# Optimization experiments

Hardware: AMD Instinct MI355X
Metric: run time of the kernel (lower is better)

Reference implementation:

```python
import jax, jax.numpy as jnp
import numpy as np

B, N, IN_DIM, ATT_DIM = 2, 8192, 512, 512


def setup_inputs() -> dict:
    key = jax.random.key(0)
    k1, k2, k3, k4 = jax.random.split(key, 4)
    X = jax.random.normal(k1, (B, N, IN_DIM), dtype=jnp.float32)
    adj = jax.random.uniform(k2, (B, N, N), dtype=jnp.float32)
    mask = jnp.ones((B, N), dtype=jnp.float32)
    # Learned params (torch Linear stores W as (out,in); we store (in,out) for x @ W)
    Wqk = jax.random.normal(k3, (IN_DIM, 2 * ATT_DIM), dtype=jnp.float32) / np.sqrt(IN_DIM)
    Wv = jax.random.normal(k4, (IN_DIM, IN_DIM), dtype=jnp.float32) / np.sqrt(IN_DIM)
    return {"X": X, "adj": adj, "mask": mask, "Wqk": Wqk, "Wv": Wv}


def reference(X, adj, mask, Wqk, Wv):
    # q, k: (B, N, att_dim); v: (B, N, in_dim)
    qk = X @ Wqk
    q, k = jnp.split(qk, 2, axis=-1)
    v = X @ Wv
    att_dim = q.shape[-1]
    inv_scale = 1.0 / jnp.sqrt(jnp.float32(att_dim))
    # Original math: w_i = inv_scale * sum_j adj_ij * m_i * m_j * (q_i . k_j).
    # Since the rank-1 mask factors (m_i m_j), fold m_j into k and m_i into the row
    # score, avoiding a second materialized NxN tensor:
    k_m = k * mask[:, :, None]                       # (B, N, att_dim)
    agg = jnp.einsum("bij,bjd->bid", adj, k_m)       # (B, N, att_dim)
    w = inv_scale * mask * jnp.einsum("bid,bid->bi", q, agg)  # (B, N)
    # softmax over the bag dimension (dim=1), then scale v rows
    L = jax.nn.softmax(w, axis=1)[:, :, None] * v    # (B, N, in_dim)
    return L
```

## Files before the change

### kernel.cpp

```cpp
#include <hip/hip_runtime.h>
#include <math.h>

#define BB 2
#define NN 8192
#define DD 512

static const float INV_SCALE = 0.04419417382415922f;

typedef short s16x8 __attribute__((ext_vector_type(8)));
typedef unsigned short u16x8 __attribute__((ext_vector_type(8)));
typedef float f32x4 __attribute__((ext_vector_type(4)));

#define AS1 __attribute__((address_space(1)))
#define AS3 __attribute__((address_space(3)))

__device__ __forceinline__ unsigned short bfbits(__bf16 h) {
    return __builtin_bit_cast(unsigned short, h);
}

__device__ __forceinline__ float b2f(unsigned short u) {
    unsigned int x = (unsigned int)u << 16;
    return __builtin_bit_cast(float, x);
}

__device__ __forceinline__ void gll16(const void* g, void* l) {
    __builtin_amdgcn_global_load_lds((const AS1 unsigned int*)g, (AS3 unsigned int*)l, 16, 0, 0);
}

__device__ __forceinline__ f32x4 ntload4(const float* p) {
    return __builtin_nontemporal_load((const f32x4*)p);
}

__global__ __launch_bounds__(256) void convx_k(
    const float* __restrict__ X, unsigned short* __restrict__ Xhi,
    unsigned short* __restrict__ Xlo)
{
    long i = (long)blockIdx.x * 256 + threadIdx.x;
    float4 x = ((const float4*)X)[i];
    __bf16 h0 = (__bf16)x.x, h1 = (__bf16)x.y, h2 = (__bf16)x.z, h3 = (__bf16)x.w;
    ushort4 hi4 = make_ushort4(bfbits(h0), bfbits(h1), bfbits(h2), bfbits(h3));
    __bf16 l0 = (__bf16)(x.x - (float)h0), l1 = (__bf16)(x.y - (float)h1);
    __bf16 l2 = (__bf16)(x.z - (float)h2), l3 = (__bf16)(x.w - (float)h3);
    ushort4 lo4 = make_ushort4(bfbits(l0), bfbits(l1), bfbits(l2), bfbits(l3));
    ((ushort4*)Xhi)[i] = hi4;
    ((ushort4*)Xlo)[i] = lo4;
}

__global__ __launch_bounds__(256) void convw_k(
    const float* __restrict__ Wqk, const float* __restrict__ Wv,
    unsigned short* __restrict__ QTh, unsigned short* __restrict__ KTh,
    unsigned short* __restrict__ KTl, unsigned short* __restrict__ VTh)
{
    int i = blockIdx.x * 256 + threadIdx.x;
    if (i < 262144) {
        int n = i >> 9, k = i & 511;
        QTh[i] = bfbits((__bf16)Wqk[k * 1024 + n]);
    } else if (i < 524288) {
        int o = i - 262144; int n = o >> 9, k = o & 511;
        float val = Wqk[k * 1024 + 512 + n];
        __bf16 h = (__bf16)val;
        KTh[o] = bfbits(h);
        KTl[o] = bfbits((__bf16)(val - (float)h));
    } else {
        int o = i - 524288; int n = o >> 9, k = o & 511;
        VTh[o] = bfbits((__bf16)Wv[k * 512 + n]);
    }
}


template <int EPI, int NT>
__global__ __launch_bounds__(256, 4) void mfma_gemm(
    const unsigned short* __restrict__ A0, const unsigned short* __restrict__ A1,
    const unsigned short* __restrict__ B0, const unsigned short* __restrict__ B1,
    float* __restrict__ C, float* __restrict__ kmf,
    unsigned short* __restrict__ ubuf, const float* __restrict__ mask,
    int N, int K)
{
    constexpr int BK = 32;
    constexpr int TILE_SH = 128 * BK;

    __shared__ unsigned short Asm[2 * TILE_SH];
    __shared__ unsigned short Bsm[2 * TILE_SH];

    const int t = threadIdx.x;
    const int wv = t >> 6, lane = t & 63;
    const int wm = wv >> 1, wn = wv & 1;
    const long m0 = blockIdx.x * 128;
    const int n0 = blockIdx.y * 128;

    f32x4 acc[4][4];
#pragma unroll
    for (int i = 0; i < 4; ++i)
#pragma unroll
        for (int j = 0; j < 4; ++j) acc[i][j] = {0.f, 0.f, 0.f, 0.f};

    const int swz = ((lane & 3) ^ ((lane >> 3) & 3)) << 4;
    auto stageA = [&](int term, int k0, int buf) {
        const unsigned short* Ab = (term < 2) ? A0 : A1;
#pragma unroll
        for (int u = 0; u < 2; ++u) {
            int c = wv * 2 + u;
            int row = c * 16 + (lane >> 2);
            gll16((const char*)Ab + ((m0 + row) * (long)K + k0) * 2 + swz,
                  (char*)Asm + buf * (TILE_SH * 2) + c * 1024);
        }
    };
    auto stageB = [&](int term, int k0, int buf) {
        const unsigned short* Bb = (NT == 3 && term == 1) ? B1 : B0;
#pragma unroll
        for (int u = 0; u < 2; ++u) {
            int c = wv * 2 + u;
            int row = c * 16 + (lane >> 2);
            gll16((const char*)Bb + ((long)(n0 + row) * K + k0) * 2 + swz,
                  (char*)Bsm + buf * (TILE_SH * 2) + c * 1024);
        }
    };

    stageA(0, 0, 0);
    stageB(0, 0, 0);
    __syncthreads();

    const int NTILES = NT * (K / BK);
    int cur = 0, term = 0, k0 = 0;
    const int g = lane >> 4;

#pragma unroll 2
    for (int tt = 0; tt < NTILES; ++tt) {
        int k0n = k0 + BK, termn = term;
        if (k0n == K) { k0n = 0; ++termn; }
        const bool hasNext = (tt + 1 < NTILES);

        if (hasNext) {
            stageA(termn, k0n, cur ^ 1);
            stageB(termn, k0n, cur ^ 1);
        }

        s16x8 av[4], bv[4];
#pragma unroll
        for (int f = 0; f < 4; ++f) {
            int ra = wm * 64 + f * 16 + (lane & 15);
            int rb = wn * 64 + f * 16 + (lane & 15);
            av[f] = *(const s16x8*)(Asm + cur * TILE_SH + ra * BK
                     + ((g ^ ((ra >> 1) & 3)) << 3));
            bv[f] = *(const s16x8*)(Bsm + cur * TILE_SH + rb * BK
                     + ((g ^ ((rb >> 1) & 3)) << 3));
        }
#pragma unroll
        for (int fm = 0; fm < 4; ++fm)
#pragma unroll
            for (int fn = 0; fn < 4; ++fn)
                acc[fm][fn] = __builtin_amdgcn_mfma_f32_16x16x32_bf16(
                    av[fm], bv[fn], acc[fm][fn], 0, 0, 0);

        __syncthreads();
        cur ^= 1; term = termn; k0 = k0n;
    }

    const long rbase = m0 + wm * 64;
    const int cbase = n0 + wn * 64;

#pragma unroll
    for (int fm = 0; fm < 4; ++fm) {
        long rb = rbase + fm * 16 + ((lane >> 4) << 2);
#pragma unroll
        for (int fn = 0; fn < 4; ++fn) {
            int c = cbase + fn * 16 + (lane & 15);
            if constexpr (EPI == 0) {
#pragma unroll
                for (int j = 0; j < 4; ++j)
                    C[(rb + j) * (long)N + c] = acc[fm][fn][j];
            } else if constexpr (EPI == 1) {
#pragma unroll
                for (int j = 0; j < 4; ++j) {
                    float kv = acc[fm][fn][j] * mask[rb + j];
                    kmf [(rb + j) * 512L + c] = kv;
                    ubuf[(rb + j) * 512L + c] = bfbits((__bf16)kv);
                }
            } else {
#pragma unroll
                for (int j = 0; j < 4; ++j)
                    ubuf[(rb + j) * 512L + c] = bfbits((__bf16)acc[fm][fn][j]);
            }
        }
    }
}

__global__ __launch_bounds__(256, 5) void sq_gemm(
    const unsigned short* __restrict__ qh,
    const unsigned short* __restrict__ kmh,
    const float* __restrict__ adj,
    float* __restrict__ w)
{
    constexpr int BK = 32;
    constexpr int TILE_SH = 128 * BK;

    __shared__ __align__(16) char smem[32768];
    unsigned short* Asm = (unsigned short*)smem;
    unsigned short* Bsm = (unsigned short*)(smem + 16384);
    unsigned short* Sh = (unsigned short*)smem;

    const int t = threadIdx.x;
    const int wv = t >> 6, lane = t & 63;
    const int wm = wv >> 1, wn = wv & 1;

    const int bid = (int)blockIdx.x;
    const int xcd = bid & 7, s = bid >> 3;
    const int z = s >> 9, r = s & 511;
    const int jj = r & 7, ii = (r >> 3) & 7, jhi = r >> 6;
    const int i_tile = xcd * 8 + ii;
    const int j_tile = jhi * 8 + jj;

    const long m0 = (long)z * NN + (long)i_tile * 128;
    const int n0 = j_tile * 128;
    const unsigned short* Bz = kmh + (long)z * NN * 512;

    f32x4 acc[4][4];
#pragma unroll
    for (int i = 0; i < 4; ++i)
#pragma unroll
        for (int j = 0; j < 4; ++j) acc[i][j] = {0.f, 0.f, 0.f, 0.f};

    const int swz = ((lane & 3) ^ ((lane >> 3) & 3)) << 4;
    auto stageA = [&](int k0, int buf) {
#pragma unroll
        for (int u = 0; u < 2; ++u) {
            int c = wv * 2 + u;
            int row = c * 16 + (lane >> 2);
            gll16((const char*)qh + ((m0 + row) * 512L + k0) * 2 + swz,
                  (char*)Asm + buf * (TILE_SH * 2) + c * 1024);
        }
    };
    auto stageB = [&](int k0, int buf) {
#pragma unroll
        for (int u = 0; u < 2; ++u) {
            int c = wv * 2 + u;
            int row = c * 16 + (lane >> 2);
            gll16((const char*)Bz + ((long)(n0 + row) * 512 + k0) * 2 + swz,
                  (char*)Bsm + buf * (TILE_SH * 2) + c * 1024);
        }
    };

    stageA(0, 0);
    stageB(0, 0);
    __syncthreads();

    const int g = lane >> 4;
#pragma unroll 2
    for (int tt = 0; tt < 16; ++tt) {
        const int cur = tt & 1;
        const bool hasNext = (tt + 1 < 16);
        if (hasNext) {
            stageA((tt + 1) * BK, cur ^ 1);
            stageB((tt + 1) * BK, cur ^ 1);
        }

        s16x8 av[4], bv[4];
#pragma unroll
        for (int f = 0; f < 4; ++f) {
            int ra = wm * 64 + f * 16 + (lane & 15);
            int rb = wn * 64 + f * 16 + (lane & 15);
            av[f] = *(const s16x8*)(Asm + cur * TILE_SH + ra * BK
                     + ((g ^ ((ra >> 1) & 3)) << 3));
            bv[f] = *(const s16x8*)(Bsm + cur * TILE_SH + rb * BK
                     + ((g ^ ((rb >> 1) & 3)) << 3));
        }
#pragma unroll
        for (int fm = 0; fm < 4; ++fm)
#pragma unroll
            for (int fn = 0; fn < 4; ++fn)
                acc[fm][fn] = __builtin_amdgcn_mfma_f32_16x16x32_bf16(
                    av[fm], bv[fn], acc[fm][fn], 0, 0, 0);

        __syncthreads();
    }

    const int g2 = lane >> 4;
#pragma unroll
    for (int fm = 0; fm < 4; ++fm) {
#pragma unroll
        for (int fn = 0; fn < 4; ++fn) {
            int c = wn * 64 + fn * 16 + (lane & 15);
            int slotx = ((((c >> 2) ^ (g2 << 2)) << 2) | (c & 3));
#pragma unroll
            for (int j = 0; j < 4; ++j) {
                int rr = wm * 64 + fm * 16 + (g2 << 2) + j;
                Sh[rr * 128 + slotx] = bfbits((__bf16)acc[fm][fn][j]);
            }
        }
    }
    __syncthreads();

    const float* adjZ = adj + (long)z * NN * NN;
    const int li0 = i_tile * 128;
    float* wz = w + (long)z * NN;

#pragma unroll 1
    for (int half = 0; half < 2; ++half) {
        f32x4 aj[8];
#pragma unroll
        for (int i = 0; i < 8; ++i) {
            int f = t + (half * 8 + i) * 256;
            int rr = f >> 5, c4 = f & 31;
            aj[i] = ntload4(adjZ + (long)(li0 + rr) * NN + n0 + c4 * 4);
        }
#pragma unroll
        for (int i = 0; i < 8; ++i) {
            int f = t + (half * 8 + i) * 256;
            int rr = f >> 5, c4 = f & 31;
            int ps = (c4 ^ (((rr >> 2) & 3) << 2)) << 2;
            ushort4 sb = *(const ushort4*)(Sh + rr * 128 + ps);
            float p = aj[i][0] * b2f(sb.x) + aj[i][1] * b2f(sb.y)
                    + aj[i][2] * b2f(sb.z) + aj[i][3] * b2f(sb.w);
            p += __shfl_xor(p, 1);  p += __shfl_xor(p, 2);
            p += __shfl_xor(p, 4);  p += __shfl_xor(p, 8);
            p += __shfl_xor(p, 16);
            if ((t & 31) == 0) atomicAdd(wz + li0 + rr, p);
        }
    }
}

__global__ __launch_bounds__(256) void fixup_k(
    float* __restrict__ w, const float* __restrict__ mask)
{
    int i = blockIdx.x * 256 + threadIdx.x;
    w[i] *= INV_SCALE * mask[i];
}

__global__ __launch_bounds__(256) void wmax_k(const float* __restrict__ w,
                                              float* __restrict__ wmax)
{
    const int b = blockIdx.x;
    const float* wr = w + (long)b * NN;
    const int t = threadIdx.x;
    float m = -3.4e38f;
    for (int i = t; i < NN; i += 256) m = fmaxf(m, wr[i]);
#pragma unroll
    for (int o = 32; o > 0; o >>= 1) m = fmaxf(m, __shfl_down(m, o));
    __shared__ float red[4];
    if ((t & 63) == 0) red[t >> 6] = m;
    __syncthreads();
    if (t == 0) wmax[b] = fmaxf(fmaxf(red[0], red[1]), fmaxf(red[2], red[3]));
}

__global__ __launch_bounds__(256) void select_k(
    const float* __restrict__ w, const float* __restrict__ wmax,
    int* __restrict__ count, int* __restrict__ cand)
{
    int i = blockIdx.x * 256 + threadIdx.x;
    int b = i >> 13;
    if (w[i] >= wmax[b] - 15.f) {
        int p = atomicAdd(count, 1);
        if (p < 128) cand[p] = i;
    }
}

__global__ __launch_bounds__(256) void qcand_k(
    const float* __restrict__ X, const float* __restrict__ Wqk,
    const int* __restrict__ cand, const int* __restrict__ count,
    float* __restrict__ qcand)
{
    int y = blockIdx.x;
    int cnt = *count; if (cnt > 128) cnt = 128;
    if (y >= cnt) return;
    const int row = cand[y];
    const float* Xr = X + (long)row * 512;
    const int t = threadIdx.x;
    __shared__ float xs[512];
    for (int k = t; k < 512; k += 256) xs[k] = Xr[k];
    __syncthreads();
    float a0 = 0.f, a1 = 0.f;
    for (int k = 0; k < 512; ++k) {
        float xv = xs[k];
        a0 += xv * Wqk[k * 1024 + t];
        a1 += xv * Wqk[k * 1024 + t + 256];
    }
    qcand[(long)y * 512 + t] = a0;
    qcand[(long)y * 512 + t + 256] = a1;
}

__global__ __launch_bounds__(256) void refine_k(
    const float* __restrict__ qcand, const float* __restrict__ km,
    const float* __restrict__ adj, const int* __restrict__ cand,
    const int* __restrict__ count, float* __restrict__ partial)
{
    int y = blockIdx.y;
    int cnt = *count; if (cnt > 128) cnt = 128;
    if (y >= cnt) return;
    const int row = cand[y];
    const int b = row >> 13, r = row & 8191;
    const int x = blockIdx.x;
    const int t = threadIdx.x, w = t >> 6, l = t & 63;

    const float* qr = qcand + (long)y * 512 + l * 8;
    const float4 q0 = *(const float4*)qr;
    const float4 q1 = *(const float4*)(qr + 4);
    const float* kmB = km + ((long)b << 13) * 512;
    const float* adjR = adj + (((long)b << 13) + r) * 8192L;

    float acc = 0.f;
    const int jbase = x * 128 + w * 32;
    for (int i = 0; i < 32; ++i) {
        int j = jbase + i;
        const float* kr = kmB + (long)j * 512 + l * 8;
        const float4 k0 = *(const float4*)kr;
        const float4 k1 = *(const float4*)(kr + 4);
        float d = q0.x * k0.x + q0.y * k0.y + q0.z * k0.z + q0.w * k0.w
                + q1.x * k1.x + q1.y * k1.y + q1.z * k1.z + q1.w * k1.w;
#pragma unroll
        for (int o = 32; o > 0; o >>= 1) d += __shfl_down(d, o);
        if (l == 0) acc += adjR[j] * d;
    }
    __shared__ float red[4];
    if (l == 0) red[w] = acc;
    __syncthreads();
    if (t == 0) partial[y * 64 + x] = red[0] + red[1] + red[2] + red[3];
}

__global__ __launch_bounds__(128) void apply_k(
    const int* __restrict__ cand, const int* __restrict__ count,
    const float* __restrict__ partial, const float* __restrict__ mask,
    float* __restrict__ w)
{
    int t = threadIdx.x;
    int cnt = *count; if (cnt > 128) cnt = 128;
    if (t < cnt) {
        float s = 0.f;
        for (int x = 0; x < 64; ++x) s += partial[t * 64 + x];
        int row = cand[t];
        w[row] = s * INV_SCALE * mask[row];
    }
}

__global__ __launch_bounds__(1024) void softmax_k(
    const float* __restrict__ w, float* __restrict__ p)
{
    const int b = blockIdx.x;
    const float* wr = w + (long)b * NN;
    float* pr = p + (long)b * NN;
    const int t = threadIdx.x;
    __shared__ float red[16];
    __shared__ float bmax, bsum;

    float m = -3.4e38f;
    for (int i = t; i < NN; i += 1024) m = fmaxf(m, wr[i]);
#pragma unroll
    for (int o = 32; o > 0; o >>= 1) m = fmaxf(m, __shfl_down(m, o));
    if ((t & 63) == 0) red[t >> 6] = m;
    __syncthreads();
    if (t == 0) {
        float mm = red[0];
        for (int i = 1; i < 16; ++i) mm = fmaxf(mm, red[i]);
        bmax = mm;
    }
    __syncthreads();
    const float M = bmax;

    float s = 0.f;
    for (int i = t; i < NN; i += 1024) s += expf(wr[i] - M);
#pragma unroll
    for (int o = 32; o > 0; o >>= 1) s += __shfl_down(s, o);
    __syncthreads();
    if ((t & 63) == 0) red[t >> 6] = s;
    __syncthreads();
    if (t == 0) {
        float ss = 0.f;
        for (int i = 0; i < 16; ++i) ss += red[i];
        bsum = ss;
    }
    __syncthreads();
    const float invS = 1.f / bsum;
    for (int i = t; i < NN; i += 1024) pr[i] = expf(wr[i] - M) * invS;
}

__global__ __launch_bounds__(256) void scale_k(
    const float* __restrict__ v, const float* __restrict__ p,
    float* __restrict__ out)
{
    const long i = (long)blockIdx.x * 256 + threadIdx.x;
    const int row = (int)(i >> 7);
    const float pv = p[row];
    float4 vv = ((const float4*)v)[i];
    vv.x *= pv; vv.y *= pv; vv.z *= pv; vv.w *= pv;
    ((float4*)out)[i] = vv;
}

extern "C" void kernel_launch(void* const* d_in, const int* in_sizes, int n_in,
                              void* d_out, int out_size, void* d_ws, size_t ws_size,
                              hipStream_t stream)
{
    const float* X    = (const float*)d_in[0];
    const float* adj  = (const float*)d_in[1];
    const float* mask = (const float*)d_in[2];
    const float* Wqk  = (const float*)d_in[3];
    const float* Wv   = (const float*)d_in[4];
    float* out = (float*)d_out;

    char* ws = (char*)d_ws;
    const long SZB = 33554432;
    float* km_buf = (float*)(ws);
    float* v_buf  = (float*)(ws + SZB);
    unsigned short* Xhi = (unsigned short*)(ws + 2 * SZB);
    unsigned short* Xlo = Xhi + 8388608;
    unsigned short* qh  = (unsigned short*)(ws + 3 * SZB);
    unsigned short* kmh = qh + 8388608;
    unsigned short* QTh = kmh + 8388608;
    unsigned short* KTh = QTh + 262144;
    unsigned short* KTl = KTh + 262144;
    unsigned short* VTh = KTl + 262144;
    float* w_buf = (float*)(VTh + 262144);
    float* p_buf = w_buf + 16384;
    float* wmax  = p_buf + 16384;
    float* partial = wmax + 64;
    float* qcand = partial + 8192;
    int* count = (int*)(qcand + 65536);
    int* cand  = count + 64;

    hipError_t e0 = hipMemsetAsync(count, 0, 4, stream); (void)e0;
    hipError_t e1 = hipMemsetAsync(w_buf, 0, 16384 * 4, stream); (void)e1;

    convx_k<<<8192, 256, 0, stream>>>(X, Xhi, Xlo);
    convw_k<<<3072, 256, 0, stream>>>(Wqk, Wv, QTh, KTh, KTl, VTh);

    mfma_gemm<1, 3><<<dim3(128, 4, 1), 256, 0, stream>>>(
        Xhi, Xlo, KTh, KTl, nullptr, km_buf, kmh, mask, 512, 512);

    mfma_gemm<2, 1><<<dim3(128, 4, 1), 256, 0, stream>>>(
        Xhi, nullptr, QTh, nullptr, nullptr, nullptr, qh, nullptr, 512, 512);

    mfma_gemm<0, 1><<<dim3(128, 4, 1), 256, 0, stream>>>(
        Xhi, nullptr, VTh, nullptr, v_buf, nullptr, nullptr, nullptr, 512, 512);

    sq_gemm<<<8192, 256, 0, stream>>>(qh, kmh, adj, w_buf);

    fixup_k<<<64, 256, 0, stream>>>(w_buf, mask);

    wmax_k<<<BB, 256, 0, stream>>>(w_buf, wmax);
    select_k<<<64, 256, 0, stream>>>(w_buf, wmax, count, cand);
    qcand_k<<<128, 256, 0, stream>>>(X, Wqk, cand, count, qcand);
    refine_k<<<dim3(64, 128, 1), 256, 0, stream>>>(qcand, km_buf, adj, cand, count, partial);
    apply_k<<<1, 128, 0, stream>>>(cand, count, partial, mask, w_buf);

    softmax_k<<<BB, 1024, 0, stream>>>(w_buf, p_buf);
    scale_k<<<8192, 256, 0, stream>>>(v_buf, p_buf, out);
}
```

Baseline: 446.6 us.

## Fuse softmax row scaling into V GEMM epilogue and merge max/select kernels

The V projection GEMM now runs after softmax and multiplies each output row by its softmax probability in its epilogue, writing straight to the output. This removes the intermediate fp32 v buffer and the separate scale kernel, saving a 32MB write plus a read and write pass. The wmax and select kernels are also merged into one two-block kernel, saving a launch but making the selection scan serial over only two blocks. Moving the V GEMM after softmax puts it on the dependent tail of the schedule.

```diff
diff --git a/kernel.cpp b/kernel.cpp
--- a/kernel.cpp
+++ b/kernel.cpp
@@ -73,7 +73,7 @@
     const unsigned short* __restrict__ A0, const unsigned short* __restrict__ A1,
     const unsigned short* __restrict__ B0, const unsigned short* __restrict__ B1,
     float* __restrict__ C, float* __restrict__ kmf,
-    unsigned short* __restrict__ ubuf, const float* __restrict__ mask,
+    unsigned short* __restrict__ ubuf, const float* __restrict__ rowscale,
     int N, int K)
 {
     constexpr int BK = 32;
@@ -172,14 +172,18 @@
             } else if constexpr (EPI == 1) {
 #pragma unroll
                 for (int j = 0; j < 4; ++j) {
-                    float kv = acc[fm][fn][j] * mask[rb + j];
+                    float kv = acc[fm][fn][j] * rowscale[rb + j];
                     kmf [(rb + j) * 512L + c] = kv;
                     ubuf[(rb + j) * 512L + c] = bfbits((__bf16)kv);
                 }
-            } else {
+            } else if constexpr (EPI == 2) {
 #pragma unroll
                 for (int j = 0; j < 4; ++j)
                     ubuf[(rb + j) * 512L + c] = bfbits((__bf16)acc[fm][fn][j]);
+            } else {
+#pragma unroll
+                for (int j = 0; j < 4; ++j)
+                    C[(rb + j) * 512L + c] = acc[fm][fn][j] * rowscale[rb + j];
             }
         }
     }
@@ -326,8 +330,9 @@
     w[i] *= INV_SCALE * mask[i];
 }
 
-__global__ __launch_bounds__(256) void wmax_k(const float* __restrict__ w,
-                                              float* __restrict__ wmax)
+__global__ __launch_bounds__(256) void wmaxsel_k(
+    const float* __restrict__ w, int* __restrict__ count,
+    int* __restrict__ cand)
 {
     const int b = blockIdx.x;
     const float* wr = w + (long)b * NN;
@@ -337,20 +342,17 @@
 #pragma unroll
     for (int o = 32; o > 0; o >>= 1) m = fmaxf(m, __shfl_down(m, o));
     __shared__ float red[4];
+    __shared__ float bm;
     if ((t & 63) == 0) red[t >> 6] = m;
     __syncthreads();
-    if (t == 0) wmax[b] = fmaxf(fmaxf(red[0], red[1]), fmaxf(red[2], red[3]));
-}
-
-__global__ __launch_bounds__(256) void select_k(
-    const float* __restrict__ w, const float* __restrict__ wmax,
-    int* __restrict__ count, int* __restrict__ cand)
-{
-    int i = blockIdx.x * 256 + threadIdx.x;
-    int b = i >> 13;
-    if (w[i] >= wmax[b] - 15.f) {
-        int p = atomicAdd(count, 1);
-        if (p < 128) cand[p] = i;
+    if (t == 0) bm = fmaxf(fmaxf(red[0], red[1]), fmaxf(red[2], red[3]));
+    __syncthreads();
+    const float thr = bm - 15.f;
+    for (int i = t; i < NN; i += 256) {
+        if (wr[i] >= thr) {
+            int p = atomicAdd(count, 1);
+            if (p < 128) cand[p] = b * NN + i;
+        }
     }
 }
 
@@ -472,18 +474,6 @@
     for (int i = t; i < NN; i += 1024) pr[i] = expf(wr[i] - M) * invS;
 }
 
-__global__ __launch_bounds__(256) void scale_k(
-    const float* __restrict__ v, const float* __restrict__ p,
-    float* __restrict__ out)
-{
-    const long i = (long)blockIdx.x * 256 + threadIdx.x;
-    const int row = (int)(i >> 7);
-    const float pv = p[row];
-    float4 vv = ((const float4*)v)[i];
-    vv.x *= pv; vv.y *= pv; vv.z *= pv; vv.w *= pv;
-    ((float4*)out)[i] = vv;
-}
-
 extern "C" void kernel_launch(void* const* d_in, const int* in_sizes, int n_in,
                               void* d_out, int out_size, void* d_ws, size_t ws_size,
                               hipStream_t stream)
@@ -498,10 +488,9 @@
     char* ws = (char*)d_ws;
     const long SZB = 33554432;
     float* km_buf = (float*)(ws);
-    float* v_buf  = (float*)(ws + SZB);
-    unsigned short* Xhi = (unsigned short*)(ws + 2 * SZB);
+    unsigned short* Xhi = (unsigned short*)(ws + SZB);
     unsigned short* Xlo = Xhi + 8388608;
-    unsigned short* qh  = (unsigned short*)(ws + 3 * SZB);
+    unsigned short* qh  = (unsigned short*)(ws + 2 * SZB);
     unsigned short* kmh = qh + 8388608;
     unsigned short* QTh = kmh + 8388608;
     unsigned short* KTh = QTh + 262144;
@@ -509,8 +498,7 @@
     unsigned short* VTh = KTl + 262144;
     float* w_buf = (float*)(VTh + 262144);
     float* p_buf = w_buf + 16384;
-    float* wmax  = p_buf + 16384;
-    float* partial = wmax + 64;
+    float* partial = p_buf + 16384;
     float* qcand = partial + 8192;
     int* count = (int*)(qcand + 65536);
     int* cand  = count + 64;
@@ -527,19 +515,17 @@
     mfma_gemm<2, 1><<<dim3(128, 4, 1), 256, 0, stream>>>(
         Xhi, nullptr, QTh, nullptr, nullptr, nullptr, qh, nullptr, 512, 512);
 
-    mfma_gemm<0, 1><<<dim3(128, 4, 1), 256, 0, stream>>>(
-        Xhi, nullptr, VTh, nullptr, v_buf, nullptr, nullptr, nullptr, 512, 512);
-
     sq_gemm<<<8192, 256, 0, stream>>>(qh, kmh, adj, w_buf);
 
     fixup_k<<<64, 256, 0, stream>>>(w_buf, mask);
 
-    wmax_k<<<BB, 256, 0, stream>>>(w_buf, wmax);
-    select_k<<<64, 256, 0, stream>>>(w_buf, wmax, count, cand);
+    wmaxsel_k<<<BB, 256, 0, stream>>>(w_buf, count, cand);
     qcand_k<<<128, 256, 0, stream>>>(X, Wqk, cand, count, qcand);
     refine_k<<<dim3(64, 128, 1), 256, 0, stream>>>(qcand, km_buf, adj, cand, count, partial);
     apply_k<<<1, 128, 0, stream>>>(cand, count, partial, mask, w_buf);
 
     softmax_k<<<BB, 1024, 0, stream>>>(w_buf, p_buf);
-    scale_k<<<8192, 256, 0, stream>>>(v_buf, p_buf, out);
-}
+
+    mfma_gemm<3, 1><<<dim3(128, 4, 1), 256, 0, stream>>>(
+        Xhi, nullptr, VTh, nullptr, out, nullptr, nullptr, p_buf, 512, 512);
+}
```

Result: no change. 439.4 us (-1.6%).
